# Kernel tuning notes

Measured on AMD Instinct MI355X. Metric: run time of the kernel, lower is better.

## Reference

```python
import jax, jax.numpy as jnp
import numpy as np

D_MODEL = 1024
NUM_HEADS = 16
GROUP_SIZE = 4
NUM_GROUPS = NUM_HEADS // GROUP_SIZE  # 4
D_K = D_MODEL // NUM_HEADS            # 64
THETA = 10000.0
WINDOW = 512


def _rope(x, positions):
    # x: (..., t, d) with d even; interleaved-pair rotation, freq_i = theta^{-i/(d/2)}
    d = x.shape[-1]
    half = d // 2
    inv_freq = THETA ** (-jnp.arange(half, dtype=x.dtype) / half)          # (half,)
    ang = positions.astype(x.dtype)[:, None] * inv_freq[None, :]           # (t, half)
    cos, sin = jnp.cos(ang), jnp.sin(ang)
    x1, x2 = x[..., 0::2], x[..., 1::2]
    r1 = x1 * cos - x2 * sin
    r2 = x1 * sin + x2 * cos
    return jnp.stack([r1, r2], axis=-1).reshape(x.shape)


def setup_inputs() -> dict:
    key = jax.random.key(0)
    k1, k2, k3, k4, k5 = jax.random.split(key, 5)
    b, t = 2, 2048
    scale = 1.0 / np.sqrt(D_MODEL)
    return {
        "x": jax.random.normal(k1, (b, t, D_MODEL), dtype=jnp.float32),
        "WQ": jax.random.normal(k2, (D_MODEL, D_MODEL), dtype=jnp.float32) * scale,
        "WK": jax.random.normal(k3, (NUM_GROUPS * D_K, D_MODEL), dtype=jnp.float32) * scale,
        "WV": jax.random.normal(k4, (NUM_GROUPS * D_K, D_MODEL), dtype=jnp.float32) * scale,
        "WO": jax.random.normal(k5, (D_MODEL, D_MODEL), dtype=jnp.float32) * scale,
        "token_positions": jnp.arange(t, dtype=jnp.int32),
    }


def reference(x, WQ, WK, WV, WO, token_positions):
    b, t, _ = x.shape
    g, s, d = NUM_GROUPS, GROUP_SIZE, D_K
    # projections (Linear: y = x @ W^T, no bias)
    q = (x @ WQ.T).reshape(b, t, g, s, d).transpose(0, 2, 3, 1, 4)  # b g s t d
    k = (x @ WK.T).reshape(b, t, g, d).transpose(0, 2, 1, 3)        # b g t d
    v = (x @ WV.T).reshape(b, t, g, d).transpose(0, 2, 1, 3)        # b g t d
    q = _rope(q, token_positions)
    k = _rope(k, token_positions)
    # scores: kv heads shared across the s query heads of each group
    scores = jnp.einsum('bgsqd,bgkd->bgsqk', q, k) / jnp.sqrt(jnp.asarray(d, x.dtype))
    i = jnp.arange(t)[:, None]
    j = jnp.arange(t)[None, :]
    allowed = (i >= j) & (i - j <= WINDOW)  # causal sliding window
    scores = jnp.where(allowed, scores, -jnp.inf)
    probs = jax.nn.softmax(scores, axis=-1)
    out = jnp.einsum('bgsqk,bgkd->bgsqd', probs, v)                 # b g s t d
    out = out.transpose(0, 3, 1, 2, 4).reshape(b, t, D_MODEL)       # b t (g s d)
    return out @ WO.T
```

## Files before the change

### kernel.cpp

```cpp
#include <hip/hip_runtime.h>
#include <hip/hip_bf16.h>

typedef __bf16 bf16;
typedef __bf16 bf16x4 __attribute__((ext_vector_type(4)));
typedef __bf16 bf16x8 __attribute__((ext_vector_type(8)));
typedef float  floatx4 __attribute__((ext_vector_type(4)));

#define D_MODEL   1024
#define NUM_HEADS 16
#define NUM_GROUPS 4
#define DK        64
#define SEQ_T     2048
#define BATCH     2
#define M_ROWS    (BATCH*SEQ_T)
#define WINDOW    512
#define KV_DIM    (NUM_GROUPS*DK)
#define N_QKV     (D_MODEL + 2*KV_DIM)
#define QSCALE    0.1803368801111204f
#define FREQ_C    0.4152410118609203f

#define GLDS16(g, l)                                                          \
    __builtin_amdgcn_global_load_lds(                                         \
        (const __attribute__((address_space(1))) void*)(g),                   \
        (__attribute__((address_space(3))) void*)(l), 16, 0, 0)

__global__ __launch_bounds__(256)
void convert_all(const float* s0, bf16* d0, int c0,
                 const float* s1, bf16* d1, int c1,
                 const float* s2, bf16* d2, int c2,
                 const float* s3, bf16* d3, int c3,
                 const float* s4, bf16* d4, int c4)
{
    int id = blockIdx.x * 256 + threadIdx.x;
    const float* src; bf16* dst;
    if      (id < c0)         { src = s0; dst = d0; }
    else if ((id -= c0) < c1) { src = s1; dst = d1; }
    else if ((id -= c1) < c2) { src = s2; dst = d2; }
    else if ((id -= c2) < c3) { src = s3; dst = d3; }
    else if ((id -= c3) < c4) { src = s4; dst = d4; }
    else return;
    int i = id * 8;
    const float* s = src + i;
    float4 a = *(const float4*)s;
    float4 b = *(const float4*)(s + 4);
    bf16x8 v;
    v[0] = (bf16)a.x; v[1] = (bf16)a.y; v[2] = (bf16)a.z; v[3] = (bf16)a.w;
    v[4] = (bf16)b.x; v[5] = (bf16)b.y; v[6] = (bf16)b.z; v[7] = (bf16)b.w;
    *(bf16x8*)&dst[i] = v;
}

__global__ __launch_bounds__(256, 3)
void gemm_t64(const bf16* __restrict__ A, const bf16* __restrict__ W, int K,
              bf16* __restrict__ Cq, bf16* __restrict__ Ck, bf16* __restrict__ Vt,
              float* __restrict__ Co, const int* __restrict__ pos, int mode)
{
    __shared__ bf16 As[2][128 * 64];
    __shared__ bf16 Bs[2][64 * 64];

    const int tid  = threadIdx.x;
    const int wave = tid >> 6;
    const int lane = tid & 63;
    const int lr   = lane & 15;
    const int quad = lane >> 4;

    const int nx    = (mode == 0) ? (N_QKV / 64) : (D_MODEL / 64);
    const int bid   = blockIdx.x;
    const int chunk = gridDim.x >> 3;
    const int v     = (bid & 7) * chunk + (bid >> 3);
    const int m0    = (v / nx) * 128;
    const int n0    = (v % nx) * 64;

    const int wm = (wave >> 1) * 64;
    const int wn = (wave & 1) * 32;

    const int cr8 = lane >> 3;
    const int cc  = ((lane & 7) ^ cr8) * 8;
    const bf16* Ag = &A[(size_t)(m0 + cr8) * K + cc];
    const bf16* Wg = &W[(size_t)(n0 + cr8) * K + cc];

#define STAGE(buf, kk)                                                        \
    do {                                                                      \
        GLDS16(Ag + (size_t)((wave * 4 + 0) * 8) * K + (kk), &As[buf][(wave * 4 + 0) * 512]); \
        GLDS16(Ag + (size_t)((wave * 4 + 1) * 8) * K + (kk), &As[buf][(wave * 4 + 1) * 512]); \
        GLDS16(Ag + (size_t)((wave * 4 + 2) * 8) * K + (kk), &As[buf][(wave * 4 + 2) * 512]); \
        GLDS16(Ag + (size_t)((wave * 4 + 3) * 8) * K + (kk), &As[buf][(wave * 4 + 3) * 512]); \
        GLDS16(Wg + (size_t)((wave * 2 + 0) * 8) * K + (kk), &Bs[buf][(wave * 2 + 0) * 512]); \
        GLDS16(Wg + (size_t)((wave * 2 + 1) * 8) * K + (kk), &Bs[buf][(wave * 2 + 1) * 512]); \
    } while (0)

    const int ax0 = (quad ^ (lane & 7)) * 8;
    const int ax1 = ax0 ^ 32;

    floatx4 acc[4][2];
#pragma unroll
    for (int i = 0; i < 4; i++)
#pragma unroll
        for (int j = 0; j < 2; j++) acc[i][j] = (floatx4)(0.0f);

    STAGE(0, 0);

    int cur = 0;
    for (int k0 = 0; k0 < K; k0 += 64) {
        if (k0 + 64 < K) {
            STAGE(cur ^ 1, k0 + 64);
            __asm__ volatile("s_waitcnt vmcnt(6)" ::: "memory");
        } else {
            __asm__ volatile("s_waitcnt vmcnt(0)" ::: "memory");
        }
        __builtin_amdgcn_s_barrier();

        bf16x8 a0[4], a1[4], b0[2], b1[2];
#pragma unroll
        for (int mi = 0; mi < 4; mi++) {
            a0[mi] = *(const bf16x8*)&As[cur][(wm + mi * 16 + lr) * 64 + ax0];
            a1[mi] = *(const bf16x8*)&As[cur][(wm + mi * 16 + lr) * 64 + ax1];
        }
#pragma unroll
        for (int ni = 0; ni < 2; ni++) {
            b0[ni] = *(const bf16x8*)&Bs[cur][(wn + ni * 16 + lr) * 64 + ax0];
            b1[ni] = *(const bf16x8*)&Bs[cur][(wn + ni * 16 + lr) * 64 + ax1];
        }

#pragma unroll
        for (int mi = 0; mi < 4; mi++)
#pragma unroll
            for (int ni = 0; ni < 2; ni++) {
                acc[mi][ni] = __builtin_amdgcn_mfma_f32_16x16x32_bf16(
                    a0[mi], b0[ni], acc[mi][ni], 0, 0, 0);
                acc[mi][ni] = __builtin_amdgcn_mfma_f32_16x16x32_bf16(
                    a1[mi], b1[ni], acc[mi][ni], 0, 0, 0);
            }

        __builtin_amdgcn_s_barrier();
        cur ^= 1;
    }
#undef STAGE

    if (mode == 0) {
        if (n0 >= D_MODEL + KV_DIM) {
            const int g  = (n0 - (D_MODEL + KV_DIM)) >> 6;
            const int b  = m0 >> 11;
            const int bg = b * 4 + g;
#pragma unroll
            for (int mi = 0; mi < 4; mi++) {
#pragma unroll
                for (int ni = 0; ni < 2; ni++) {
                    int d  = wn + ni * 16 + lr;
                    int t0 = (m0 & (SEQ_T - 1)) + wm + mi * 16 + quad * 4;
                    bf16x4 vv;
#pragma unroll
                    for (int r = 0; r < 4; r++) vv[r] = (bf16)acc[mi][ni][r];
                    *(bf16x4*)&Vt[((size_t)(bg * 64 + d)) * SEQ_T + t0] = vv;
                }
            }
        } else {
            bf16* out; int ld, coff; float sc;
            if (n0 < D_MODEL) { out = Cq; ld = D_MODEL; coff = n0; sc = QSCALE; }
            else              { out = Ck; ld = KV_DIM;  coff = n0 - D_MODEL; sc = 1.0f; }
            float inv[2];
            float sgn = (lr & 1) ? 1.0f : -1.0f;
#pragma unroll
            for (int ni = 0; ni < 2; ni++) {
                int ip = (wn + ni * 16 + lr) >> 1;
                inv[ni] = exp2f(-(float)ip * FREQ_C);
            }
#pragma unroll
            for (int mi = 0; mi < 4; mi++) {
#pragma unroll
                for (int r = 0; r < 4; r++) {
                    int row = m0 + wm + mi * 16 + quad * 4 + r;
                    float p = (float)pos[row & (SEQ_T - 1)];
#pragma unroll
                    for (int ni = 0; ni < 2; ni++) {
                        float vv = acc[mi][ni][r];
                        float vp = __shfl_xor(vv, 1);
                        float ang = p * inv[ni];
                        float ss, cc2;
                        __sincosf(ang, &ss, &cc2);
                        vv = vv * cc2 + vp * ss * sgn;
                        out[(size_t)row * ld + coff + wn + ni * 16 + lr] = (bf16)(vv * sc);
                    }
                }
            }
        }
    } else {
#pragma unroll
        for (int mi = 0; mi < 4; mi++)
#pragma unroll
            for (int ni = 0; ni < 2; ni++)
#pragma unroll
                for (int r = 0; r < 4; r++) {
                    int row = m0 + wm + mi * 16 + quad * 4 + r;
                    int col = n0 + wn + ni * 16 + lr;
                    Co[(size_t)row * D_MODEL + col] = acc[mi][ni][r];
                }
    }
}

__global__ __launch_bounds__(256)
void attn_mfma(const bf16* __restrict__ Q, const bf16* __restrict__ K,
               const bf16* __restrict__ Vt_g, bf16* __restrict__ AO)
{
    const int ST = 72;
    __shared__ bf16 Ks[64 * ST];
    __shared__ bf16 Vt[80 * ST];

    const int tid  = threadIdx.x;
    const int wave = tid >> 6;
    const int lane = tid & 63;
    const int lr   = lane & 15;
    const int quad = lane >> 4;
    const int bg = blockIdx.y;
    const int b = bg >> 2, g = bg & 3;
    const int h = g * 4 + wave;
    const int q0 = blockIdx.x * 32;

    bf16x8 qf[2][2];
#pragma unroll
    for (int mi = 0; mi < 2; mi++)
#pragma unroll
        for (int ks = 0; ks < 2; ks++)
            qf[mi][ks] = *(const bf16x8*)
                &Q[((size_t)(b * SEQ_T + q0 + mi * 16 + lr)) * D_MODEL
                   + h * 64 + ks * 32 + quad * 8];

    for (int i = tid; i < 15 * ST; i += 256) Vt[65 * ST + i] = (bf16)0.0f;
    if (tid < ST) Vt[64 * ST + tid] = (bf16)(tid < 64 ? 1.0f : 0.0f);

    floatx4 o[2][5];
#pragma unroll
    for (int mi = 0; mi < 2; mi++)
#pragma unroll
        for (int nt = 0; nt < 5; nt++) o[mi][nt] = (floatx4)(0.0f);

    const int t0   = (q0 >= WINDOW) ? ((q0 - WINDOW) & ~63) : 0;
    const int last = q0 & ~63;

    const int srow0 = tid >> 3,         scol0 = (tid & 7) * 8;
    const int srow1 = (tid + 256) >> 3, scol1 = ((tid + 256) & 7) * 8;

    const int wc0 = scol0 & 31;
    const int w00 = (scol0 & ~31) + ((wc0 & 15) >> 2) * 8 + (wc0 >> 4) * 4;
    const int wc1 = scol1 & 31;
    const int w10 = (scol1 & ~31) + ((wc1 & 15) >> 2) * 8 + (wc1 >> 4) * 4;

    bf16x8 kreg[2], vreg[2];
#define LOADKV(jn)                                                            \
    do {                                                                      \
        kreg[0] = *(const bf16x8*)&K[((size_t)(b * SEQ_T + (jn) + srow0)) * KV_DIM + g * 64 + scol0]; \
        vreg[0] = *(const bf16x8*)&Vt_g[((size_t)(bg * 64 + srow0)) * SEQ_T + (jn) + scol0];          \
        kreg[1] = *(const bf16x8*)&K[((size_t)(b * SEQ_T + (jn) + srow1)) * KV_DIM + g * 64 + scol1]; \
        vreg[1] = *(const bf16x8*)&Vt_g[((size_t)(bg * 64 + srow1)) * SEQ_T + (jn) + scol1];          \
    } while (0)

    LOADKV(t0);

    for (int j0 = t0; j0 <= last; j0 += 64) {
        const bool mC = (j0 == last);
        const bool mW = (q0 >= WINDOW) && (j0 == t0);
        __syncthreads();
        *(bf16x8*)&Ks[srow0 * ST + scol0] = kreg[0];
        *(bf16x8*)&Ks[srow1 * ST + scol1] = kreg[1];
        *(bf16x4*)&Vt[srow0 * ST + w00] =
            __builtin_shufflevector(vreg[0], vreg[0], 0, 1, 2, 3);
        *(bf16x4*)&Vt[srow0 * ST + w00 + 8] =
            __builtin_shufflevector(vreg[0], vreg[0], 4, 5, 6, 7);
        *(bf16x4*)&Vt[srow1 * ST + w10] =
            __builtin_shufflevector(vreg[1], vreg[1], 0, 1, 2, 3);
        *(bf16x4*)&Vt[srow1 * ST + w10 + 8] =
            __builtin_shufflevector(vreg[1], vreg[1], 4, 5, 6, 7);
        if (j0 + 64 <= last) LOADKV(j0 + 64);
        __syncthreads();

        floatx4 s2[4][2];
#pragma unroll
        for (int nt = 0; nt < 4; nt++)
#pragma unroll
            for (int mi = 0; mi < 2; mi++) s2[nt][mi] = (floatx4)(0.0f);
#pragma unroll
        for (int ks = 0; ks < 2; ks++) {
#pragma unroll
            for (int nt = 0; nt < 4; nt++) {
                bf16x8 kf = *(const bf16x8*)&Ks[(nt * 16 + lr) * ST + ks * 32 + quad * 8];
                s2[nt][0] = __builtin_amdgcn_mfma_f32_16x16x32_bf16(kf, qf[0][ks], s2[nt][0], 0, 0, 0);
                s2[nt][1] = __builtin_amdgcn_mfma_f32_16x16x32_bf16(kf, qf[1][ks], s2[nt][1], 0, 0, 0);
            }
        }

        if (mC) {
#pragma unroll
            for (int nt = 0; nt < 4; nt++)
#pragma unroll
                for (int mi = 0; mi < 2; mi++) {
                    int qi_ = q0 + mi * 16 + lr;
#pragma unroll
                    for (int r = 0; r < 4; r++) {
                        int key = j0 + nt * 16 + quad * 4 + r;
                        s2[nt][mi][r] = (key <= qi_) ? s2[nt][mi][r] : -1e30f;
                    }
                }
        } else if (mW) {
#pragma unroll
            for (int nt = 0; nt < 4; nt++)
#pragma unroll
                for (int mi = 0; mi < 2; mi++) {
                    int qi_ = q0 + mi * 16 + lr;
#pragma unroll
                    for (int r = 0; r < 4; r++) {
                        int key = j0 + nt * 16 + quad * 4 + r;
                        s2[nt][mi][r] = (qi_ - key <= WINDOW) ? s2[nt][mi][r] : -1e30f;
                    }
                }
        }

        bf16x8 pa[2][2];
#pragma unroll
        for (int mi = 0; mi < 2; mi++)
#pragma unroll
            for (int ks = 0; ks < 2; ks++)
#pragma unroll
                for (int r = 0; r < 4; r++) {
                    pa[mi][ks][r]     = (bf16)exp2f(s2[2 * ks][mi][r]);
                    pa[mi][ks][r + 4] = (bf16)exp2f(s2[2 * ks + 1][mi][r]);
                }

#pragma unroll
        for (int ks = 0; ks < 2; ks++) {
#pragma unroll
            for (int nt = 0; nt < 5; nt++) {
                bf16x8 vf = *(const bf16x8*)&Vt[(nt * 16 + lr) * ST + ks * 32 + quad * 8];
                o[0][nt] = __builtin_amdgcn_mfma_f32_16x16x32_bf16(pa[0][ks], vf, o[0][nt], 0, 0, 0);
                o[1][nt] = __builtin_amdgcn_mfma_f32_16x16x32_bf16(pa[1][ks], vf, o[1][nt], 0, 0, 0);
            }
        }
    }
#undef LOADKV

#pragma unroll
    for (int mi = 0; mi < 2; mi++)
#pragma unroll
        for (int r = 0; r < 4; r++) {
            float l = __shfl(o[mi][4][r], lane & 48);
            float invl = 1.0f / l;
            int row = q0 + mi * 16 + quad * 4 + r;
#pragma unroll
            for (int nt = 0; nt < 4; nt++)
                AO[((size_t)(b * SEQ_T + row)) * D_MODEL + h * 64 + nt * 16 + lr] =
                    (bf16)(o[mi][nt][r] * invl);
        }
}

extern "C" void kernel_launch(void* const* d_in, const int* in_sizes, int n_in,
                              void* d_out, int out_size, void* d_ws, size_t ws_size,
                              hipStream_t stream)
{
    const float* x  = (const float*)d_in[0];
    const float* WQ = (const float*)d_in[1];
    const float* WK = (const float*)d_in[2];
    const float* WV = (const float*)d_in[3];
    const float* WO = (const float*)d_in[4];
    const int*  pos = (const int*)d_in[5];

    char* ws   = (char*)d_ws;
    bf16* Qw   = (bf16*)ws;
    bf16* Kw   = (bf16*)(ws + (size_t) 8 * 1024 * 1024);
    bf16* Vt_g = (bf16*)(ws + (size_t)10 * 1024 * 1024);
    bf16* xb   = (bf16*)(ws + (size_t)12 * 1024 * 1024);
    bf16* AO   = xb;
    bf16* Wqkv = (bf16*)(ws + (size_t)20 * 1024 * 1024);
    bf16* WOb  = (bf16*)(ws + (size_t)23 * 1024 * 1024);

    const int cx = (M_ROWS * D_MODEL) / 8;
    const int cq = (D_MODEL * D_MODEL) / 8;
    const int ck = (KV_DIM * D_MODEL) / 8;
    const int ctot = cx + cq + 2 * ck + cq;
    convert_all<<<ctot / 256, 256, 0, stream>>>(
        x, xb, cx,
        WQ, Wqkv, cq,
        WK, Wqkv + (size_t)D_MODEL * D_MODEL, ck,
        WV, Wqkv + (size_t)(D_MODEL + KV_DIM) * D_MODEL, ck,
        WO, WOb, cq);

    gemm_t64<<<(N_QKV / 64) * (M_ROWS / 128), 256, 0, stream>>>(
        xb, Wqkv, D_MODEL, Qw, Kw, Vt_g, nullptr, pos, 0);

    attn_mfma<<<dim3(SEQ_T / 32, BATCH * NUM_GROUPS), 256, 0, stream>>>(
        Qw, Kw, Vt_g, AO);

    gemm_t64<<<(D_MODEL / 64) * (M_ROWS / 128), 256, 0, stream>>>(
        AO, WOb, D_MODEL, nullptr, nullptr, nullptr, (float*)d_out, pos, 1);
}
```

Baseline: 139.8 us.

## Enlarge GEMM tiles to 128x128 and drop LDS double buffering

The projection GEMM tile grows from 128x64 to 128x128, with each wave computing a 64x64 sub-tile (4x4 MFMA accumulators). Double buffering is removed: each k-step loads one tile, waits for it fully, then computes. The epilogue now uses a per-wave column offset so the RoPE, Q/K and V-transpose routing works with the wider tile. This raises data reuse per loaded byte and halves the grid size, but global loads no longer overlap with MFMA work and fewer blocks are left to fill the CUs.

New measurement: 150.8 us. +7.9%, slower.

```diff
diff --git a/kernel.cpp b/kernel.cpp
--- a/kernel.cpp
+++ b/kernel.cpp
@@ -49,13 +49,13 @@
     *(bf16x8*)&dst[i] = v;
 }
 
-__global__ __launch_bounds__(256, 3)
+__global__ __launch_bounds__(256)
 void gemm_t64(const bf16* __restrict__ A, const bf16* __restrict__ W, int K,
               bf16* __restrict__ Cq, bf16* __restrict__ Ck, bf16* __restrict__ Vt,
               float* __restrict__ Co, const int* __restrict__ pos, int mode)
 {
-    __shared__ bf16 As[2][128 * 64];
-    __shared__ bf16 Bs[2][64 * 64];
+    __shared__ bf16 As[128 * 64];
+    __shared__ bf16 Bs[128 * 64];
 
     const int tid  = threadIdx.x;
     const int wave = tid >> 6;
@@ -63,68 +63,63 @@
     const int lr   = lane & 15;
     const int quad = lane >> 4;
 
-    const int nx    = (mode == 0) ? (N_QKV / 64) : (D_MODEL / 64);
+    const int nx    = (mode == 0) ? (N_QKV / 128) : (D_MODEL / 128);
     const int bid   = blockIdx.x;
     const int chunk = gridDim.x >> 3;
     const int v     = (bid & 7) * chunk + (bid >> 3);
     const int m0    = (v / nx) * 128;
-    const int n0    = (v % nx) * 64;
+    const int n0    = (v % nx) * 128;
 
     const int wm = (wave >> 1) * 64;
-    const int wn = (wave & 1) * 32;
+    const int wn = (wave & 1) * 64;
 
     const int cr8 = lane >> 3;
     const int cc  = ((lane & 7) ^ cr8) * 8;
     const bf16* Ag = &A[(size_t)(m0 + cr8) * K + cc];
     const bf16* Wg = &W[(size_t)(n0 + cr8) * K + cc];
 
-#define STAGE(buf, kk)                                                        \
+#define STAGE(kk)                                                             \
     do {                                                                      \
-        GLDS16(Ag + (size_t)((wave * 4 + 0) * 8) * K + (kk), &As[buf][(wave * 4 + 0) * 512]); \
-        GLDS16(Ag + (size_t)((wave * 4 + 1) * 8) * K + (kk), &As[buf][(wave * 4 + 1) * 512]); \
-        GLDS16(Ag + (size_t)((wave * 4 + 2) * 8) * K + (kk), &As[buf][(wave * 4 + 2) * 512]); \
-        GLDS16(Ag + (size_t)((wave * 4 + 3) * 8) * K + (kk), &As[buf][(wave * 4 + 3) * 512]); \
-        GLDS16(Wg + (size_t)((wave * 2 + 0) * 8) * K + (kk), &Bs[buf][(wave * 2 + 0) * 512]); \
-        GLDS16(Wg + (size_t)((wave * 2 + 1) * 8) * K + (kk), &Bs[buf][(wave * 2 + 1) * 512]); \
+        GLDS16(Ag + (size_t)((wave * 4 + 0) * 8) * K + (kk), &As[(wave * 4 + 0) * 512]); \
+        GLDS16(Ag + (size_t)((wave * 4 + 1) * 8) * K + (kk), &As[(wave * 4 + 1) * 512]); \
+        GLDS16(Ag + (size_t)((wave * 4 + 2) * 8) * K + (kk), &As[(wave * 4 + 2) * 512]); \
+        GLDS16(Ag + (size_t)((wave * 4 + 3) * 8) * K + (kk), &As[(wave * 4 + 3) * 512]); \
+        GLDS16(Wg + (size_t)((wave * 4 + 0) * 8) * K + (kk), &Bs[(wave * 4 + 0) * 512]); \
+        GLDS16(Wg + (size_t)((wave * 4 + 1) * 8) * K + (kk), &Bs[(wave * 4 + 1) * 512]); \
+        GLDS16(Wg + (size_t)((wave * 4 + 2) * 8) * K + (kk), &Bs[(wave * 4 + 2) * 512]); \
+        GLDS16(Wg + (size_t)((wave * 4 + 3) * 8) * K + (kk), &Bs[(wave * 4 + 3) * 512]); \
     } while (0)
 
     const int ax0 = (quad ^ (lane & 7)) * 8;
     const int ax1 = ax0 ^ 32;
 
-    floatx4 acc[4][2];
+    floatx4 acc[4][4];
 #pragma unroll
     for (int i = 0; i < 4; i++)
 #pragma unroll
-        for (int j = 0; j < 2; j++) acc[i][j] = (floatx4)(0.0f);
-
-    STAGE(0, 0);
-
-    int cur = 0;
+        for (int j = 0; j < 4; j++) acc[i][j] = (floatx4)(0.0f);
+
     for (int k0 = 0; k0 < K; k0 += 64) {
-        if (k0 + 64 < K) {
-            STAGE(cur ^ 1, k0 + 64);
-            __asm__ volatile("s_waitcnt vmcnt(6)" ::: "memory");
-        } else {
-            __asm__ volatile("s_waitcnt vmcnt(0)" ::: "memory");
-        }
+        STAGE(k0);
+        __asm__ volatile("s_waitcnt vmcnt(0)" ::: "memory");
         __builtin_amdgcn_s_barrier();
 
-        bf16x8 a0[4], a1[4], b0[2], b1[2];
+        bf16x8 a0[4], a1[4], b0[4], b1[4];
 #pragma unroll
         for (int mi = 0; mi < 4; mi++) {
-            a0[mi] = *(const bf16x8*)&As[cur][(wm + mi * 16 + lr) * 64 + ax0];
-            a1[mi] = *(const bf16x8*)&As[cur][(wm + mi * 16 + lr) * 64 + ax1];
-        }
-#pragma unroll
-        for (int ni = 0; ni < 2; ni++) {
-            b0[ni] = *(const bf16x8*)&Bs[cur][(wn + ni * 16 + lr) * 64 + ax0];
-            b1[ni] = *(const bf16x8*)&Bs[cur][(wn + ni * 16 + lr) * 64 + ax1];
+            a0[mi] = *(const bf16x8*)&As[(wm + mi * 16 + lr) * 64 + ax0];
+            a1[mi] = *(const bf16x8*)&As[(wm + mi * 16 + lr) * 64 + ax1];
+        }
+#pragma unroll
+        for (int ni = 0; ni < 4; ni++) {
+            b0[ni] = *(const bf16x8*)&Bs[(wn + ni * 16 + lr) * 64 + ax0];
+            b1[ni] = *(const bf16x8*)&Bs[(wn + ni * 16 + lr) * 64 + ax1];
         }
 
 #pragma unroll
         for (int mi = 0; mi < 4; mi++)
 #pragma unroll
-            for (int ni = 0; ni < 2; ni++) {
+            for (int ni = 0; ni < 4; ni++) {
                 acc[mi][ni] = __builtin_amdgcn_mfma_f32_16x16x32_bf16(
                     a0[mi], b0[ni], acc[mi][ni], 0, 0, 0);
                 acc[mi][ni] = __builtin_amdgcn_mfma_f32_16x16x32_bf16(
@@ -132,20 +127,20 @@
             }
 
         __builtin_amdgcn_s_barrier();
-        cur ^= 1;
     }
 #undef STAGE
 
     if (mode == 0) {
-        if (n0 >= D_MODEL + KV_DIM) {
-            const int g  = (n0 - (D_MODEL + KV_DIM)) >> 6;
+        const int nw = n0 + wn;
+        if (nw >= D_MODEL + KV_DIM) {
+            const int g  = (nw - (D_MODEL + KV_DIM)) >> 6;
             const int b  = m0 >> 11;
             const int bg = b * 4 + g;
 #pragma unroll
             for (int mi = 0; mi < 4; mi++) {
 #pragma unroll
-                for (int ni = 0; ni < 2; ni++) {
-                    int d  = wn + ni * 16 + lr;
+                for (int ni = 0; ni < 4; ni++) {
+                    int d  = ni * 16 + lr;
                     int t0 = (m0 & (SEQ_T - 1)) + wm + mi * 16 + quad * 4;
                     bf16x4 vv;
 #pragma unroll
@@ -155,13 +150,13 @@
             }
         } else {
             bf16* out; int ld, coff; float sc;
-            if (n0 < D_MODEL) { out = Cq; ld = D_MODEL; coff = n0; sc = QSCALE; }
-            else              { out = Ck; ld = KV_DIM;  coff = n0 - D_MODEL; sc = 1.0f; }
-            float inv[2];
+            if (nw < D_MODEL) { out = Cq; ld = D_MODEL; coff = nw; sc = QSCALE; }
+            else              { out = Ck; ld = KV_DIM;  coff = nw - D_MODEL; sc = 1.0f; }
+            float inv[4];
             float sgn = (lr & 1) ? 1.0f : -1.0f;
 #pragma unroll
-            for (int ni = 0; ni < 2; ni++) {
-                int ip = (wn + ni * 16 + lr) >> 1;
+            for (int ni = 0; ni < 4; ni++) {
+                int ip = (ni * 16 + lr) >> 1;
                 inv[ni] = exp2f(-(float)ip * FREQ_C);
             }
 #pragma unroll
@@ -171,14 +166,14 @@
                     int row = m0 + wm + mi * 16 + quad * 4 + r;
                     float p = (float)pos[row & (SEQ_T - 1)];
 #pragma unroll
-                    for (int ni = 0; ni < 2; ni++) {
+                    for (int ni = 0; ni < 4; ni++) {
                         float vv = acc[mi][ni][r];
                         float vp = __shfl_xor(vv, 1);
                         float ang = p * inv[ni];
                         float ss, cc2;
                         __sincosf(ang, &ss, &cc2);
                         vv = vv * cc2 + vp * ss * sgn;
-                        out[(size_t)row * ld + coff + wn + ni * 16 + lr] = (bf16)(vv * sc);
+                        out[(size_t)row * ld + coff + ni * 16 + lr] = (bf16)(vv * sc);
                     }
                 }
             }
@@ -187,7 +182,7 @@
 #pragma unroll
         for (int mi = 0; mi < 4; mi++)
 #pragma unroll
-            for (int ni = 0; ni < 2; ni++)
+            for (int ni = 0; ni < 4; ni++)
 #pragma unroll
                 for (int r = 0; r < 4; r++) {
                     int row = m0 + wm + mi * 16 + quad * 4 + r;
@@ -381,12 +376,12 @@
         WV, Wqkv + (size_t)(D_MODEL + KV_DIM) * D_MODEL, ck,
         WO, WOb, cq);
 
-    gemm_t64<<<(N_QKV / 64) * (M_ROWS / 128), 256, 0, stream>>>(
+    gemm_t64<<<(N_QKV / 128) * (M_ROWS / 128), 256, 0, stream>>>(
         xb, Wqkv, D_MODEL, Qw, Kw, Vt_g, nullptr, pos, 0);
 
     attn_mfma<<<dim3(SEQ_T / 32, BATCH * NUM_GROUPS), 256, 0, stream>>>(
         Qw, Kw, Vt_g, AO);
 
-    gemm_t64<<<(D_MODEL / 64) * (M_ROWS / 128), 256, 0, stream>>>(
+    gemm_t64<<<(D_MODEL / 128) * (M_ROWS / 128), 256, 0, stream>>>(
         AO, WOb, D_MODEL, nullptr, nullptr, nullptr, (float*)d_out, pos, 1);
 }
```
